# Kernel tuning notes

Hardware: AMD Instinct MI355X
Metric: run time of the kernel (lower is better)

The kernel has to match this reference:

```python
import jax, jax.numpy as jnp
import numpy as np

B, S, D = 16, 1024, 512
H, DH = 8, 64  # heads, dim_head


def setup_inputs() -> dict:
    key = jax.random.key(0)
    ks = jax.random.split(key, 7)
    x = jax.random.normal(ks[0], (B, S, D), dtype=jnp.float32)
    # variable sequence lengths in [1, S]
    seq_lens = jnp.maximum(jax.random.randint(ks[1], (B,), 0, S + 1), 1).astype(jnp.int32)
    w_std = 0.02
    Wq = jax.random.normal(ks[2], (D, D), dtype=jnp.float32) * w_std
    Wk = jax.random.normal(ks[3], (D, D), dtype=jnp.float32) * w_std
    Wv = jax.random.normal(ks[4], (D, D), dtype=jnp.float32) * w_std
    Wo = jax.random.normal(ks[5], (D, D), dtype=jnp.float32) * w_std
    bo = jnp.zeros((D,), dtype=jnp.float32)
    return {"x": x, "seq_lens": seq_lens, "Wq": Wq, "Wk": Wk, "Wv": Wv, "Wo": Wo, "bo": bo}


def reference(x, seq_lens, Wq, Wk, Wv, Wo, bo):
    # x: [B, S, D] padded ragged batch; seq_lens: [B] valid token counts.
    # Equivalent to the per-batch SDPA loop over jagged sequences: attention
    # is computed only among the valid tokens of each sequence.
    scale = DH ** -0.5
    q = (x @ Wq).reshape(B, S, H, DH)
    k = (x @ Wk).reshape(B, S, H, DH)
    v = (x @ Wv).reshape(B, S, H, DH)
    scores = jnp.einsum('bqhd,bkhd->bhqk', q, k) * scale  # [B,H,S,S]
    valid = jnp.arange(S)[None, :] < seq_lens[:, None]     # [B,S] token mask
    neg_inf = jnp.finfo(scores.dtype).min
    scores = jnp.where(valid[:, None, None, :], scores, neg_inf)
    attn = jax.nn.softmax(scores, axis=-1)
    out = jnp.einsum('bhqk,bkhd->bqhd', attn, v).reshape(B, S, D)
    out = out @ Wo + bo  # to_out Linear (dropout=0 / eval)
    return out * valid[:, :, None]  # zero padded query positions
```

## Files before the change

### kernel.cpp

```cpp
#include <hip/hip_runtime.h>
#include <hip/hip_bf16.h>

typedef __bf16 bf16_t;
typedef __attribute__((ext_vector_type(4))) __bf16 bf16x4;
typedef __attribute__((ext_vector_type(8))) __bf16 bf16x8;
typedef __attribute__((ext_vector_type(4))) float f32x4;

#define MFMA16(a, b, c) __builtin_amdgcn_mfma_f32_16x16x32_bf16((a), (b), (c), 0, 0, 0)

#define BB 16
#define SS 1024
#define DD 512
#define HH 8
#define DH 64
#define NTOK (BB * SS)
#define QSCALE 0.18033688f

typedef const __attribute__((address_space(1))) void gas_void;
typedef __attribute__((address_space(3))) void las_void;

__device__ __forceinline__ void async_cp16(const void* g, void* l) {
    __builtin_amdgcn_global_load_lds((gas_void*)g, (las_void*)l, 16, 0, 0);
}

__device__ __forceinline__ bf16x8 frag_ld(const char* sm, int row, int kk, int g) {
    int r7 = row & 7;
    int base = row * 128 + ((g & 1) << 3);
    int c0 = ((kk << 2) + (g >> 1)) ^ r7;
    int c1 = ((kk << 2) + 2 + (g >> 1)) ^ r7;
    bf16x4 lo = *(const bf16x4*)(sm + base + (c0 << 4));
    bf16x4 hi = *(const bf16x4*)(sm + base + (c1 << 4));
    return __builtin_shufflevector(lo, hi, 0, 1, 2, 3, 4, 5, 6, 7);
}

__device__ __forceinline__ bf16x8 fragl(const char* sm, int idx, int l) {
    return *(const bf16x8*)(sm + (idx * 64 + l) * 16);
}

__global__ __launch_bounds__(256) void cast_x_k(const float* __restrict__ x,
                                                bf16_t* __restrict__ xb, int n4) {
    int i = blockIdx.x * 256 + threadIdx.x;
    if (i < n4) {
        float4 v = ((const float4*)x)[i];
        bf16x4 o;
        o[0] = (bf16_t)v.x; o[1] = (bf16_t)v.y; o[2] = (bf16_t)v.z; o[3] = (bf16_t)v.w;
        *(bf16x4*)(xb + (size_t)i * 4) = o;
    }
}

__global__ __launch_bounds__(256) void transpose_w_k(const float* __restrict__ W0,
                                                     const float* __restrict__ W1,
                                                     const float* __restrict__ W2,
                                                     const float* __restrict__ W3,
                                                     bf16_t* __restrict__ Wt) {
    __shared__ float t[32][33];
    int z = blockIdx.z;
    const float* W = (z == 0) ? W0 : (z == 1) ? W1 : (z == 2) ? W2 : W3;
    bf16_t* out = Wt + (size_t)z * DD * DD;
    int n0 = blockIdx.x * 32, k0 = blockIdx.y * 32;
    int tx = threadIdx.x, ty = threadIdx.y;
#pragma unroll
    for (int i = 0; i < 32; i += 8)
        t[ty + i][tx] = W[(size_t)(k0 + ty + i) * DD + n0 + tx];
    __syncthreads();
#pragma unroll
    for (int i = 0; i < 32; i += 8)
        out[(size_t)(n0 + ty + i) * DD + k0 + tx] = (bf16_t)t[tx][ty + i];
}

__global__ void build_q_k(const int* __restrict__ sl, ushort* __restrict__ items,
                          int* __restrict__ meta) {
    int l = threadIdx.x;
    __shared__ int s_b[BB], s_cnt[BB], s_start[BB];
    if (l < BB) {
        int len = sl[l];
        int rank = 0;
        for (int j = 0; j < BB; ++j) {
            int lj = sl[j];
            if (lj > len || (lj == len && j < l)) ++rank;
        }
        s_b[rank] = l;
        s_cnt[rank] = ((len + 127) >> 7) * HH;
    }
    __syncthreads();
    if (l < BB) {
        int st = 0;
        for (int j = 0; j < l; ++j) st += s_cnt[j];
        s_start[l] = st;
        if (l == BB - 1) { meta[0] = st + s_cnt[l]; meta[1] = 0; }
    }
    __syncthreads();
    if (l < BB) {
        int b = s_b[l], st = s_start[l], c = s_cnt[l];
        int nqt = c >> 3;
        for (int i = 0; i < c; ++i) {
            int h = i / nqt, qt = i - h * nqt;
            items[st + i] = (ushort)((((b << 3) | h) << 3) | qt);
        }
    }
}

template <int MODE>
__global__ __launch_bounds__(256) void gemm_k(const bf16_t* __restrict__ A,
                                              const bf16_t* __restrict__ WtBase,
                                              bf16_t* __restrict__ oQ,
                                              bf16_t* __restrict__ oK,
                                              bf16_t* __restrict__ oVt,
                                              float* __restrict__ oO,
                                              const float* __restrict__ bo,
                                              const int* __restrict__ seq_lens) {
    __shared__ __align__(16) char smem[32768];
    char* smA = smem;
    char* smB = smem + 16384;
    const int tid = threadIdx.x;
    const int l = tid & 63, w = tid >> 6;
    const int lr = l & 15, g = l >> 4;
    const int bm = blockIdx.x, bn = blockIdx.y;
    const int z = (MODE == 0) ? blockIdx.z : 3;
    const bf16_t* Wt = WtBase + (size_t)z * DD * DD;
    const int row0 = bm * 128;
    const int col0 = bn * 128;
    const int wm = (w >> 1) * 64, wn = (w & 1) * 64;

    f32x4 acc[4][4] = {};

    for (int kt = 0; kt < 8; ++kt) {
        const int k0 = kt * 64;
        __syncthreads();
#pragma unroll
        for (int it = 0; it < 4; ++it) {
            int cl = it * 256 + tid;
            int m = cl >> 3, p = cl & 7, c = p ^ (m & 7);
            async_cp16(A + (size_t)(row0 + m) * DD + k0 + c * 8, smA + cl * 16);
        }
#pragma unroll
        for (int it = 0; it < 4; ++it) {
            int cl = it * 256 + tid;
            int m = cl >> 3, p = cl & 7, c = p ^ (m & 7);
            async_cp16(Wt + (size_t)(col0 + m) * DD + k0 + c * 8, smB + cl * 16);
        }
        __syncthreads();
#pragma unroll
        for (int kk = 0; kk < 2; ++kk) {
            bf16x8 af[4], bfr[4];
#pragma unroll
            for (int i = 0; i < 4; ++i) af[i] = frag_ld(smA, wm + i * 16 + lr, kk, g);
#pragma unroll
            for (int j = 0; j < 4; ++j) bfr[j] = frag_ld(smB, wn + j * 16 + lr, kk, g);
#pragma unroll
            for (int i = 0; i < 4; ++i)
#pragma unroll
                for (int j = 0; j < 4; ++j)
                    acc[i][j] = MFMA16(af[i], bfr[j], acc[i][j]);
        }
    }

    if (MODE == 0) {
        __syncthreads();
        char* tl = smem;
        const float sc = (z == 0) ? QSCALE : 1.f;
#pragma unroll
        for (int i = 0; i < 4; ++i)
#pragma unroll
            for (int j = 0; j < 4; ++j)
#pragma unroll
                for (int r = 0; r < 4; ++r) {
                    int s = wm + i * 16 + g * 4 + r;
                    int n = wn + j * 16 + lr;
                    int nb = 2 * n;
                    int byte = s * 256 + ((((nb >> 4) ^ (s & 7)) << 4) | (nb & 15));
                    *(bf16_t*)(tl + byte) = (bf16_t)(acc[i][j][r] * sc);
                }
        __syncthreads();
        const int b = row0 >> 10, s0 = row0 & 1023;
        if (z < 2) {
            bf16_t* dst = (z == 0) ? oQ : oK;
#pragma unroll
            for (int c8 = 0; c8 < 8; ++c8) {
                int combo = c8 * 4 + w;
                int kk = combo & 1, t = (combo >> 1) & 7, hl = combo >> 4;
                int s = 16 * t + lr;
                bf16x4 pr[2];
#pragma unroll
                for (int jj = 0; jj < 2; ++jj) {
                    int nb = 128 * hl + 64 * kk + 32 * jj + 8 * g;
                    int byte = s * 256 + ((((nb >> 4) ^ (s & 7)) << 4) | (nb & 15));
                    pr[jj] = *(const bf16x4*)(tl + byte);
                }
                bf16x8 v = __builtin_shufflevector(pr[0], pr[1], 0, 1, 2, 3, 4, 5, 6, 7);
                int bhh = b * 8 + (col0 >> 6) + hl;
                int tg = (s0 >> 4) + t;
                *(bf16x8*)(dst + (((size_t)bhh * 64 + tg) * 2 + kk) * 512 + l * 8) = v;
            }
        } else {
#pragma unroll
            for (int c8 = 0; c8 < 8; ++c8) {
                int combo = c8 * 4 + w;
                int kk = combo & 1, dt = (combo >> 1) & 3;
                int st = (combo >> 3) & 1, hl = (combo >> 4) & 1;
                bf16x8 v;
#pragma unroll
                for (int j = 0; j < 8; ++j) {
                    int s = 64 * st + 32 * kk + 16 * (j >> 2) + 4 * g + (j & 3);
                    int n = 64 * hl + 16 * dt + lr;
                    int nb = 2 * n;
                    int byte = s * 256 + ((((nb >> 4) ^ (s & 7)) << 4) | (nb & 15));
                    v[j] = *(const bf16_t*)(tl + byte);
                }
                int bhh = b * 8 + (col0 >> 6) + hl;
                int stg = (s0 >> 6) + st;
                *(bf16x8*)(oVt + ((((size_t)bhh * 16 + stg) * 4 + dt) * 2 + kk) * 512 +
                           l * 8) = v;
            }
        }
    } else {
        int b = row0 >> 10;
        int len = seq_lens[b];
#pragma unroll
        for (int i = 0; i < 4; ++i) {
            int mrow = row0 + wm + i * 16 + g * 4;
#pragma unroll
            for (int j = 0; j < 4; ++j) {
                int n = col0 + wn + j * 16 + lr;
                float bias = bo[n];
#pragma unroll
                for (int r = 0; r < 4; ++r) {
                    int m = mrow + r;
                    int s = m & 1023;
                    oO[(size_t)m * DD + n] = (s < len) ? (acc[i][j][r] + bias) : 0.f;
                }
            }
        }
    }
}

__global__ __launch_bounds__(256) void attn_k(const bf16_t* __restrict__ Qf,
                                              const bf16_t* __restrict__ Kf,
                                              const bf16_t* __restrict__ Vf,
                                              bf16_t* __restrict__ O,
                                              const int* __restrict__ seq_lens,
                                              const ushort* __restrict__ items,
                                              int* __restrict__ meta) {
    __shared__ __align__(16) char smem[49152];
    __shared__ int s_item;
    const int tid = threadIdx.x, l = tid & 63, w = tid >> 6;
    const int lr = l & 15, g = l >> 4;
    const int nitems = meta[0];
    int* cursor = meta + 1;

    for (;;) {
        if (tid == 0) s_item = atomicAdd(cursor, 1);
        __syncthreads();
        const int ii = s_item;
        if (ii >= nitems) return;
        const int itv = items[ii];
        const int qt = itv & 7, bh = itv >> 3;
        const int b = bh >> 3;
        const int len = seq_lens[b];
        const int q0 = qt * 128;
        const int h = bh & 7;

        const bf16_t* kfb = Kf + (size_t)bh * 65536;
        const bf16_t* vfb = Vf + (size_t)bh * 65536;

        bf16x8 bq[2][2];
#pragma unroll
        for (int qs = 0; qs < 2; ++qs) {
            int t = (q0 >> 4) + 2 * w + qs;
#pragma unroll
            for (int kk = 0; kk < 2; ++kk)
                bq[qs][kk] = *(const bf16x8*)(
                    Qf + (((size_t)bh * 64 + t) * 2 + kk) * 512 + l * 8);
        }

        f32x4 oacc[2][4] = {};
        float mrun[2] = {-1e30f, -1e30f};
        float lpart[2] = {0.f, 0.f};

        const int nkt = (len + 63) >> 6;

        auto stage = [&](int buf, int kti) {
            char* smK = smem + buf * 16384;
            char* smV = smK + 8192;
            const bf16_t* ks = kfb + kti * 4096;
            const bf16_t* vs = vfb + kti * 4096;
#pragma unroll
            for (int it = 0; it < 2; ++it) {
                int cl = it * 256 + tid;
                async_cp16(ks + cl * 8, smK + cl * 16);
            }
#pragma unroll
            for (int it = 0; it < 2; ++it) {
                int cl = it * 256 + tid;
                async_cp16(vs + cl * 8, smV + cl * 16);
            }
        };

        stage(0, 0);
        if (nkt > 1) stage(1, 1);
        int cur = 0;

        for (int kt = 0; kt < nkt; ++kt) {
            const int key0 = kt * 64;
            if (kt + 1 < nkt) {
                asm volatile("s_waitcnt vmcnt(4)" ::: "memory");
            } else {
                asm volatile("s_waitcnt vmcnt(0)" ::: "memory");
            }
            __builtin_amdgcn_s_barrier();
            __builtin_amdgcn_sched_barrier(0);
            if (kt + 2 < nkt) {
                int b2 = (cur >= 1) ? cur - 1 : 2;
                stage(b2, kt + 2);
            }
            const char* smK = smem + cur * 16384;
            const char* smV = smK + 8192;

            bf16x8 bv[4][2];
#pragma unroll
            for (int dt = 0; dt < 4; ++dt)
#pragma unroll
                for (int kk = 0; kk < 2; ++kk)
                    bv[dt][kk] = fragl(smV, dt * 2 + kk, l);

            f32x4 pacc[2][4] = {};
#pragma unroll
            for (int nt = 0; nt < 4; ++nt) {
                bf16x8 ak0 = fragl(smK, nt * 2 + 0, l);
                bf16x8 ak1 = fragl(smK, nt * 2 + 1, l);
#pragma unroll
                for (int qs = 0; qs < 2; ++qs) {
                    pacc[qs][nt] = MFMA16(ak0, bq[qs][0], pacc[qs][nt]);
                    pacc[qs][nt] = MFMA16(ak1, bq[qs][1], pacc[qs][nt]);
                }
            }

            const bool full = (key0 + 64 <= len);

#pragma unroll
            for (int qs = 0; qs < 2; ++qs) {
                float mloc = -1e30f;
                if (full) {
#pragma unroll
                    for (int nt = 0; nt < 4; ++nt)
#pragma unroll
                        for (int r = 0; r < 4; ++r) mloc = fmaxf(mloc, pacc[qs][nt][r]);
                } else {
#pragma unroll
                    for (int nt = 0; nt < 4; ++nt)
#pragma unroll
                        for (int r = 0; r < 4; ++r) {
                            int kg = key0 + nt * 16 + 4 * g + r;
                            float s = (kg < len) ? pacc[qs][nt][r] : -1e30f;
                            pacc[qs][nt][r] = s;
                            mloc = fmaxf(mloc, s);
                        }
                }
                mloc = fmaxf(mloc, __shfl_xor(mloc, 16, 64));
                mloc = fmaxf(mloc, __shfl_xor(mloc, 32, 64));

                float mn;
                if (__all(mloc <= mrun[qs])) {
                    mn = mrun[qs];
                } else {
                    mn = fmaxf(mrun[qs], mloc);
                    float corr = __builtin_amdgcn_exp2f(mrun[qs] - mn);
                    mrun[qs] = mn;
                    lpart[qs] *= corr;
                    float cb[4];
#pragma unroll
                    for (int r = 0; r < 4; ++r) cb[r] = __shfl(corr, 4 * g + r, 64);
#pragma unroll
                    for (int dt = 0; dt < 4; ++dt)
#pragma unroll
                        for (int r = 0; r < 4; ++r) oacc[qs][dt][r] *= cb[r];
                }

                float ls = 0.f;
#pragma unroll
                for (int nt = 0; nt < 4; ++nt)
#pragma unroll
                    for (int r = 0; r < 4; ++r) {
                        float p = __builtin_amdgcn_exp2f(pacc[qs][nt][r] - mn);
                        pacc[qs][nt][r] = p;
                        ls += p;
                    }
                lpart[qs] += ls;

                bf16x8 pa[2];
#pragma unroll
                for (int kf = 0; kf < 2; ++kf)
#pragma unroll
                    for (int j = 0; j < 8; ++j)
                        pa[kf][j] = (bf16_t)pacc[qs][2 * kf + (j >> 2)][j & 3];
#pragma unroll
                for (int kf = 0; kf < 2; ++kf)
#pragma unroll
                    for (int dt = 0; dt < 4; ++dt)
                        oacc[qs][dt] = MFMA16(pa[kf], bv[dt][kf], oacc[qs][dt]);
            }
            cur = (cur == 2) ? 0 : cur + 1;
        }

#pragma unroll
        for (int qs = 0; qs < 2; ++qs) {
            float lt = lpart[qs];
            lt += __shfl_xor(lt, 16, 64);
            lt += __shfl_xor(lt, 32, 64);
#pragma unroll
            for (int r = 0; r < 4; ++r) {
                float inv = 1.f / __shfl(lt, 4 * g + r, 64);
                int q = q0 + w * 32 + qs * 16 + 4 * g + r;
                size_t orow = ((size_t)b * SS + q) * DD;
#pragma unroll
                for (int dt = 0; dt < 4; ++dt)
                    O[orow + h * DH + dt * 16 + lr] = (bf16_t)(oacc[qs][dt][r] * inv);
            }
        }
    }
}

extern "C" void kernel_launch(void* const* d_in, const int* in_sizes, int n_in,
                              void* d_out, int out_size, void* d_ws, size_t ws_size,
                              hipStream_t stream) {
    const float* x = (const float*)d_in[0];
    const int* seq_lens = (const int*)d_in[1];
    const float* Wq = (const float*)d_in[2];
    const float* Wk = (const float*)d_in[3];
    const float* Wv = (const float*)d_in[4];
    const float* Wo = (const float*)d_in[5];
    const float* bo = (const float*)d_in[6];
    float* out = (float*)d_out;

    char* ws = (char*)d_ws;
    const size_t SEG = (size_t)NTOK * DD * sizeof(bf16_t);
    bf16_t* xb = (bf16_t*)ws;
    bf16_t* qb = (bf16_t*)(ws + SEG);
    bf16_t* kb = (bf16_t*)(ws + 2 * SEG);
    bf16_t* vtb = (bf16_t*)(ws + 3 * SEG);
    bf16_t* wt = (bf16_t*)(ws + 4 * SEG);
    ushort* items = (ushort*)(ws + 4 * SEG + (size_t)4 * DD * DD * sizeof(bf16_t));
    int* meta = (int*)(items + 1024);
    bf16_t* ab = xb;

    build_q_k<<<dim3(1), dim3(64), 0, stream>>>(seq_lens, items, meta);
    cast_x_k<<<dim3((NTOK * DD / 4) / 256), dim3(256), 0, stream>>>(x, xb, NTOK * DD / 4);
    transpose_w_k<<<dim3(16, 16, 4), dim3(32, 8), 0, stream>>>(Wq, Wk, Wv, Wo, wt);
    gemm_k<0><<<dim3(NTOK / 128, DD / 128, 3), dim3(256), 0, stream>>>(
        xb, wt, qb, kb, vtb, nullptr, nullptr, nullptr);
    attn_k<<<dim3(768), dim3(256), 0, stream>>>(qb, kb, vtb, ab, seq_lens, items, meta);
    gemm_k<2><<<dim3(NTOK / 128, DD / 128, 1), dim3(256), 0, stream>>>(
        ab, wt, nullptr, nullptr, nullptr, out, bo, seq_lens);
}
```

Baseline: 122.6 us.

## Make attention work items per-wave 32-query tiles with direct global K/V loads

The attention kernel now treats each wavefront as an independent worker. It pulls 32-query work items from the atomic queue with a wave-level shuffle instead of a block barrier, and reads K/V fragments straight from global memory into registers, dropping the LDS triple-buffered async staging. The finer items are meant to improve load balance across ragged sequence lengths and remove block-wide synchronisation. In exchange, K/V tiles are no longer shared across four waves through LDS, so global/L2 traffic roughly quadruples and load latency is no longer hidden by the prefetch pipeline.

Result: slower. 160.3 us (+30.8%).

```diff
diff --git a/kernel.cpp b/kernel.cpp
--- a/kernel.cpp
+++ b/kernel.cpp
@@ -31,10 +31,6 @@
     bf16x4 lo = *(const bf16x4*)(sm + base + (c0 << 4));
     bf16x4 hi = *(const bf16x4*)(sm + base + (c1 << 4));
     return __builtin_shufflevector(lo, hi, 0, 1, 2, 3, 4, 5, 6, 7);
-}
-
-__device__ __forceinline__ bf16x8 fragl(const char* sm, int idx, int l) {
-    return *(const bf16x8*)(sm + (idx * 64 + l) * 16);
 }
 
 __global__ __launch_bounds__(256) void cast_x_k(const float* __restrict__ x,
@@ -80,7 +76,7 @@
             if (lj > len || (lj == len && j < l)) ++rank;
         }
         s_b[rank] = l;
-        s_cnt[rank] = ((len + 127) >> 7) * HH;
+        s_cnt[rank] = ((len + 31) >> 5) * HH;
     }
     __syncthreads();
     if (l < BB) {
@@ -92,10 +88,10 @@
     __syncthreads();
     if (l < BB) {
         int b = s_b[l], st = s_start[l], c = s_cnt[l];
-        int nqt = c >> 3;
+        int nq32 = c >> 3;
         for (int i = 0; i < c; ++i) {
-            int h = i / nqt, qt = i - h * nqt;
-            items[st + i] = (ushort)((((b << 3) | h) << 3) | qt);
+            int h = i / nq32, qt = i - h * nq32;
+            items[st + i] = (ushort)((((b << 3) | h) << 5) | qt);
         }
     }
 }
@@ -241,37 +237,32 @@
                                               const int* __restrict__ seq_lens,
                                               const ushort* __restrict__ items,
                                               int* __restrict__ meta) {
-    __shared__ __align__(16) char smem[49152];
-    __shared__ int s_item;
-    const int tid = threadIdx.x, l = tid & 63, w = tid >> 6;
+    const int tid = threadIdx.x, l = tid & 63;
     const int lr = l & 15, g = l >> 4;
     const int nitems = meta[0];
     int* cursor = meta + 1;
 
     for (;;) {
-        if (tid == 0) s_item = atomicAdd(cursor, 1);
-        __syncthreads();
-        const int ii = s_item;
+        int v = 0;
+        if (l == 0) v = atomicAdd(cursor, 1);
+        const int ii = __shfl(v, 0, 64);
         if (ii >= nitems) return;
         const int itv = items[ii];
-        const int qt = itv & 7, bh = itv >> 3;
-        const int b = bh >> 3;
+        const int qt = itv & 31, bh = itv >> 5;
+        const int b = bh >> 3, h = bh & 7;
         const int len = seq_lens[b];
-        const int q0 = qt * 128;
-        const int h = bh & 7;
+        const int q0 = qt * 32;
 
         const bf16_t* kfb = Kf + (size_t)bh * 65536;
         const bf16_t* vfb = Vf + (size_t)bh * 65536;
 
         bf16x8 bq[2][2];
 #pragma unroll
-        for (int qs = 0; qs < 2; ++qs) {
-            int t = (q0 >> 4) + 2 * w + qs;
+        for (int qs = 0; qs < 2; ++qs)
 #pragma unroll
             for (int kk = 0; kk < 2; ++kk)
                 bq[qs][kk] = *(const bf16x8*)(
-                    Qf + (((size_t)bh * 64 + t) * 2 + kk) * 512 + l * 8);
-        }
+                    Qf + (((size_t)bh * 64 + (q0 >> 4) + qs) * 2 + kk) * 512 + l * 8);
 
         f32x4 oacc[2][4] = {};
         float mrun[2] = {-1e30f, -1e30f};
@@ -279,61 +270,32 @@
 
         const int nkt = (len + 63) >> 6;
 
-        auto stage = [&](int buf, int kti) {
-            char* smK = smem + buf * 16384;
-            char* smV = smK + 8192;
-            const bf16_t* ks = kfb + kti * 4096;
-            const bf16_t* vs = vfb + kti * 4096;
-#pragma unroll
-            for (int it = 0; it < 2; ++it) {
-                int cl = it * 256 + tid;
-                async_cp16(ks + cl * 8, smK + cl * 16);
-            }
-#pragma unroll
-            for (int it = 0; it < 2; ++it) {
-                int cl = it * 256 + tid;
-                async_cp16(vs + cl * 8, smV + cl * 16);
-            }
-        };
-
-        stage(0, 0);
-        if (nkt > 1) stage(1, 1);
-        int cur = 0;
-
         for (int kt = 0; kt < nkt; ++kt) {
             const int key0 = kt * 64;
-            if (kt + 1 < nkt) {
-                asm volatile("s_waitcnt vmcnt(4)" ::: "memory");
-            } else {
-                asm volatile("s_waitcnt vmcnt(0)" ::: "memory");
-            }
-            __builtin_amdgcn_s_barrier();
-            __builtin_amdgcn_sched_barrier(0);
-            if (kt + 2 < nkt) {
-                int b2 = (cur >= 1) ? cur - 1 : 2;
-                stage(b2, kt + 2);
-            }
-            const char* smK = smem + cur * 16384;
-            const char* smV = smK + 8192;
+            bf16x8 ak[4][2];
+#pragma unroll
+            for (int nt = 0; nt < 4; ++nt)
+#pragma unroll
+                for (int kk = 0; kk < 2; ++kk)
+                    ak[nt][kk] = *(const bf16x8*)(
+                        kfb + (size_t)((kt * 4 + nt) * 2 + kk) * 512 + l * 8);
+
+            f32x4 pacc[2][4] = {};
+#pragma unroll
+            for (int nt = 0; nt < 4; ++nt)
+#pragma unroll
+                for (int qs = 0; qs < 2; ++qs) {
+                    pacc[qs][nt] = MFMA16(ak[nt][0], bq[qs][0], pacc[qs][nt]);
+                    pacc[qs][nt] = MFMA16(ak[nt][1], bq[qs][1], pacc[qs][nt]);
+                }
 
             bf16x8 bv[4][2];
 #pragma unroll
             for (int dt = 0; dt < 4; ++dt)
 #pragma unroll
                 for (int kk = 0; kk < 2; ++kk)
-                    bv[dt][kk] = fragl(smV, dt * 2 + kk, l);
-
-            f32x4 pacc[2][4] = {};
-#pragma unroll
-            for (int nt = 0; nt < 4; ++nt) {
-                bf16x8 ak0 = fragl(smK, nt * 2 + 0, l);
-                bf16x8 ak1 = fragl(smK, nt * 2 + 1, l);
-#pragma unroll
-                for (int qs = 0; qs < 2; ++qs) {
-                    pacc[qs][nt] = MFMA16(ak0, bq[qs][0], pacc[qs][nt]);
-                    pacc[qs][nt] = MFMA16(ak1, bq[qs][1], pacc[qs][nt]);
-                }
-            }
+                    bv[dt][kk] = *(const bf16x8*)(
+                        vfb + (size_t)((kt * 8) + dt * 2 + kk) * 512 + l * 8);
 
             const bool full = (key0 + 64 <= len);
 
@@ -399,7 +361,6 @@
                     for (int dt = 0; dt < 4; ++dt)
                         oacc[qs][dt] = MFMA16(pa[kf], bv[dt][kf], oacc[qs][dt]);
             }
-            cur = (cur == 2) ? 0 : cur + 1;
         }
 
 #pragma unroll
@@ -410,7 +371,7 @@
 #pragma unroll
             for (int r = 0; r < 4; ++r) {
                 float inv = 1.f / __shfl(lt, 4 * g + r, 64);
-                int q = q0 + w * 32 + qs * 16 + 4 * g + r;
+                int q = q0 + qs * 16 + 4 * g + r;
                 size_t orow = ((size_t)b * SS + q) * DD;
 #pragma unroll
                 for (int dt = 0; dt < 4; ++dt)
@@ -440,7 +401,7 @@
     bf16_t* vtb = (bf16_t*)(ws + 3 * SEG);
     bf16_t* wt = (bf16_t*)(ws + 4 * SEG);
     ushort* items = (ushort*)(ws + 4 * SEG + (size_t)4 * DD * DD * sizeof(bf16_t));
-    int* meta = (int*)(items + 1024);
+    int* meta = (int*)(items + 4096);
     bf16_t* ab = xb;
 
     build_q_k<<<dim3(1), dim3(64), 0, stream>>>(seq_lens, items, meta);
@@ -448,7 +409,7 @@
     transpose_w_k<<<dim3(16, 16, 4), dim3(32, 8), 0, stream>>>(Wq, Wk, Wv, Wo, wt);
     gemm_k<0><<<dim3(NTOK / 128, DD / 128, 3), dim3(256), 0, stream>>>(
         xb, wt, qb, kb, vtb, nullptr, nullptr, nullptr);
-    attn_k<<<dim3(768), dim3(256), 0, stream>>>(qb, kb, vtb, ab, seq_lens, items, meta);
+    attn_k<<<dim3(512), dim3(256), 0, stream>>>(qb, kb, vtb, ab, seq_lens, items, meta);
     gemm_k<2><<<dim3(NTOK / 128, DD / 128, 1), dim3(256), 0, stream>>>(
         ab, wt, nullptr, nullptr, nullptr, out, bo, seq_lens);
 }
```

## Shrink attention query tile to 64 rows, double-buffer K/V, lazy rescale

Applied to the files above, without the earlier changes.

Attention work items now cover 64 query rows per head (16 per wave) instead of 128, so the persistent scheduler has finer-grained items and less padding for ragged lengths, and the grid grows to 1280 blocks. K/V staging moves from a 3-deep to a 2-deep LDS ring with full waitcnt, which cuts shared memory to 32 KB but exposes more load latency. The online softmax now rescales only when the new max exceeds the running max by more than 8 (in log2 units), which skips correction work but lets exponentials grow up to 2^8 before normalization. Each wave now reuses every K/V fragment read from LDS for only one 16-row query tile instead of two, raising LDS traffic per FLOP.

Measured after the change: 126.4 us. 3.1% more time.

```diff
diff --git a/kernel.cpp b/kernel.cpp
--- a/kernel.cpp
+++ b/kernel.cpp
@@ -80,7 +80,7 @@
             if (lj > len || (lj == len && j < l)) ++rank;
         }
         s_b[rank] = l;
-        s_cnt[rank] = ((len + 127) >> 7) * HH;
+        s_cnt[rank] = ((len + 63) >> 6) * HH;
     }
     __syncthreads();
     if (l < BB) {
@@ -92,10 +92,10 @@
     __syncthreads();
     if (l < BB) {
         int b = s_b[l], st = s_start[l], c = s_cnt[l];
-        int nqt = c >> 3;
+        int nq = c >> 3;
         for (int i = 0; i < c; ++i) {
-            int h = i / nqt, qt = i - h * nqt;
-            items[st + i] = (ushort)((((b << 3) | h) << 3) | qt);
+            int h = i / nq, qt = i - h * nq;
+            items[st + i] = (ushort)((((b << 3) | h) << 4) | qt);
         }
     }
 }
@@ -241,7 +241,7 @@
                                               const int* __restrict__ seq_lens,
                                               const ushort* __restrict__ items,
                                               int* __restrict__ meta) {
-    __shared__ __align__(16) char smem[49152];
+    __shared__ __align__(16) char smem[32768];
     __shared__ int s_item;
     const int tid = threadIdx.x, l = tid & 63, w = tid >> 6;
     const int lr = l & 15, g = l >> 4;
@@ -254,28 +254,23 @@
         const int ii = s_item;
         if (ii >= nitems) return;
         const int itv = items[ii];
-        const int qt = itv & 7, bh = itv >> 3;
-        const int b = bh >> 3;
+        const int qt = itv & 15, bh = itv >> 4;
+        const int b = bh >> 3, h = bh & 7;
         const int len = seq_lens[b];
-        const int q0 = qt * 128;
-        const int h = bh & 7;
+        const int q0 = qt * 64 + w * 16;
 
         const bf16_t* kfb = Kf + (size_t)bh * 65536;
         const bf16_t* vfb = Vf + (size_t)bh * 65536;
 
-        bf16x8 bq[2][2];
-#pragma unroll
-        for (int qs = 0; qs < 2; ++qs) {
-            int t = (q0 >> 4) + 2 * w + qs;
-#pragma unroll
-            for (int kk = 0; kk < 2; ++kk)
-                bq[qs][kk] = *(const bf16x8*)(
-                    Qf + (((size_t)bh * 64 + t) * 2 + kk) * 512 + l * 8);
-        }
-
-        f32x4 oacc[2][4] = {};
-        float mrun[2] = {-1e30f, -1e30f};
-        float lpart[2] = {0.f, 0.f};
+        bf16x8 bq[2];
+        {
+            size_t tb = ((size_t)bh * 64 + (q0 >> 4)) * 2;
+            bq[0] = *(const bf16x8*)(Qf + (tb + 0) * 512 + l * 8);
+            bq[1] = *(const bf16x8*)(Qf + (tb + 1) * 512 + l * 8);
+        }
+
+        f32x4 oacc[4] = {};
+        float mrun = -1e30f, lpart = 0.f;
 
         const int nkt = (len + 63) >> 6;
 
@@ -284,137 +279,107 @@
             char* smV = smK + 8192;
             const bf16_t* ks = kfb + kti * 4096;
             const bf16_t* vs = vfb + kti * 4096;
-#pragma unroll
-            for (int it = 0; it < 2; ++it) {
-                int cl = it * 256 + tid;
-                async_cp16(ks + cl * 8, smK + cl * 16);
-            }
-#pragma unroll
-            for (int it = 0; it < 2; ++it) {
-                int cl = it * 256 + tid;
-                async_cp16(vs + cl * 8, smV + cl * 16);
-            }
+            async_cp16(ks + tid * 8, smK + tid * 16);
+            async_cp16(ks + (256 + tid) * 8, smK + (256 + tid) * 16);
+            async_cp16(vs + tid * 8, smV + tid * 16);
+            async_cp16(vs + (256 + tid) * 8, smV + (256 + tid) * 16);
         };
 
         stage(0, 0);
-        if (nkt > 1) stage(1, 1);
         int cur = 0;
 
         for (int kt = 0; kt < nkt; ++kt) {
             const int key0 = kt * 64;
-            if (kt + 1 < nkt) {
-                asm volatile("s_waitcnt vmcnt(4)" ::: "memory");
-            } else {
-                asm volatile("s_waitcnt vmcnt(0)" ::: "memory");
-            }
+            asm volatile("s_waitcnt vmcnt(0)" ::: "memory");
             __builtin_amdgcn_s_barrier();
-            __builtin_amdgcn_sched_barrier(0);
-            if (kt + 2 < nkt) {
-                int b2 = (cur >= 1) ? cur - 1 : 2;
-                stage(b2, kt + 2);
-            }
+            if (kt + 1 < nkt) stage(cur ^ 1, kt + 1);
             const char* smK = smem + cur * 16384;
             const char* smV = smK + 8192;
 
-            bf16x8 bv[4][2];
-#pragma unroll
-            for (int dt = 0; dt < 4; ++dt)
-#pragma unroll
-                for (int kk = 0; kk < 2; ++kk)
-                    bv[dt][kk] = fragl(smV, dt * 2 + kk, l);
-
-            f32x4 pacc[2][4] = {};
+            f32x4 pacc[4] = {};
 #pragma unroll
             for (int nt = 0; nt < 4; ++nt) {
                 bf16x8 ak0 = fragl(smK, nt * 2 + 0, l);
                 bf16x8 ak1 = fragl(smK, nt * 2 + 1, l);
-#pragma unroll
-                for (int qs = 0; qs < 2; ++qs) {
-                    pacc[qs][nt] = MFMA16(ak0, bq[qs][0], pacc[qs][nt]);
-                    pacc[qs][nt] = MFMA16(ak1, bq[qs][1], pacc[qs][nt]);
-                }
+                pacc[nt] = MFMA16(ak0, bq[0], pacc[nt]);
+                pacc[nt] = MFMA16(ak1, bq[1], pacc[nt]);
             }
 
             const bool full = (key0 + 64 <= len);
 
-#pragma unroll
-            for (int qs = 0; qs < 2; ++qs) {
-                float mloc = -1e30f;
-                if (full) {
-#pragma unroll
-                    for (int nt = 0; nt < 4; ++nt)
-#pragma unroll
-                        for (int r = 0; r < 4; ++r) mloc = fmaxf(mloc, pacc[qs][nt][r]);
-                } else {
-#pragma unroll
-                    for (int nt = 0; nt < 4; ++nt)
-#pragma unroll
-                        for (int r = 0; r < 4; ++r) {
-                            int kg = key0 + nt * 16 + 4 * g + r;
-                            float s = (kg < len) ? pacc[qs][nt][r] : -1e30f;
-                            pacc[qs][nt][r] = s;
-                            mloc = fmaxf(mloc, s);
-                        }
-                }
-                mloc = fmaxf(mloc, __shfl_xor(mloc, 16, 64));
-                mloc = fmaxf(mloc, __shfl_xor(mloc, 32, 64));
-
-                float mn;
-                if (__all(mloc <= mrun[qs])) {
-                    mn = mrun[qs];
-                } else {
-                    mn = fmaxf(mrun[qs], mloc);
-                    float corr = __builtin_amdgcn_exp2f(mrun[qs] - mn);
-                    mrun[qs] = mn;
-                    lpart[qs] *= corr;
-                    float cb[4];
-#pragma unroll
-                    for (int r = 0; r < 4; ++r) cb[r] = __shfl(corr, 4 * g + r, 64);
-#pragma unroll
-                    for (int dt = 0; dt < 4; ++dt)
-#pragma unroll
-                        for (int r = 0; r < 4; ++r) oacc[qs][dt][r] *= cb[r];
-                }
-
-                float ls = 0.f;
+            float mloc = -1e30f;
+            if (full) {
 #pragma unroll
                 for (int nt = 0; nt < 4; ++nt)
 #pragma unroll
+                    for (int r = 0; r < 4; ++r) mloc = fmaxf(mloc, pacc[nt][r]);
+            } else {
+#pragma unroll
+                for (int nt = 0; nt < 4; ++nt)
+#pragma unroll
                     for (int r = 0; r < 4; ++r) {
-                        float p = __builtin_amdgcn_exp2f(pacc[qs][nt][r] - mn);
-                        pacc[qs][nt][r] = p;
-                        ls += p;
+                        int kg = key0 + nt * 16 + 4 * g + r;
+                        float s = (kg < len) ? pacc[nt][r] : -1e30f;
+                        pacc[nt][r] = s;
+                        mloc = fmaxf(mloc, s);
                     }
-                lpart[qs] += ls;
-
-                bf16x8 pa[2];
-#pragma unroll
-                for (int kf = 0; kf < 2; ++kf)
-#pragma unroll
-                    for (int j = 0; j < 8; ++j)
-                        pa[kf][j] = (bf16_t)pacc[qs][2 * kf + (j >> 2)][j & 3];
-#pragma unroll
-                for (int kf = 0; kf < 2; ++kf)
-#pragma unroll
-                    for (int dt = 0; dt < 4; ++dt)
-                        oacc[qs][dt] = MFMA16(pa[kf], bv[dt][kf], oacc[qs][dt]);
-            }
-            cur = (cur == 2) ? 0 : cur + 1;
-        }
-
-#pragma unroll
-        for (int qs = 0; qs < 2; ++qs) {
-            float lt = lpart[qs];
+            }
+            mloc = fmaxf(mloc, __shfl_xor(mloc, 16, 64));
+            mloc = fmaxf(mloc, __shfl_xor(mloc, 32, 64));
+
+            if (!__all(mloc <= mrun + 8.f)) {
+                float mn = fmaxf(mrun, mloc);
+                float corr = __builtin_amdgcn_exp2f(mrun - mn);
+                mrun = mn;
+                lpart *= corr;
+                float cb[4];
+#pragma unroll
+                for (int r = 0; r < 4; ++r) cb[r] = __shfl(corr, 4 * g + r, 64);
+#pragma unroll
+                for (int dt = 0; dt < 4; ++dt)
+#pragma unroll
+                    for (int r = 0; r < 4; ++r) oacc[dt][r] *= cb[r];
+            }
+
+            float ls = 0.f;
+#pragma unroll
+            for (int nt = 0; nt < 4; ++nt)
+#pragma unroll
+                for (int r = 0; r < 4; ++r) {
+                    float p = __builtin_amdgcn_exp2f(pacc[nt][r] - mrun);
+                    pacc[nt][r] = p;
+                    ls += p;
+                }
+            lpart += ls;
+
+            bf16x8 pa[2];
+#pragma unroll
+            for (int kf = 0; kf < 2; ++kf)
+#pragma unroll
+                for (int j = 0; j < 8; ++j)
+                    pa[kf][j] = (bf16_t)pacc[2 * kf + (j >> 2)][j & 3];
+#pragma unroll
+            for (int kf = 0; kf < 2; ++kf)
+#pragma unroll
+                for (int dt = 0; dt < 4; ++dt) {
+                    bf16x8 bv = fragl(smV, dt * 2 + kf, l);
+                    oacc[dt] = MFMA16(pa[kf], bv, oacc[dt]);
+                }
+            cur ^= 1;
+        }
+
+        {
+            float lt = lpart;
             lt += __shfl_xor(lt, 16, 64);
             lt += __shfl_xor(lt, 32, 64);
 #pragma unroll
             for (int r = 0; r < 4; ++r) {
                 float inv = 1.f / __shfl(lt, 4 * g + r, 64);
-                int q = q0 + w * 32 + qs * 16 + 4 * g + r;
+                int q = q0 + 4 * g + r;
                 size_t orow = ((size_t)b * SS + q) * DD;
 #pragma unroll
                 for (int dt = 0; dt < 4; ++dt)
-                    O[orow + h * DH + dt * 16 + lr] = (bf16_t)(oacc[qs][dt][r] * inv);
+                    O[orow + h * DH + dt * 16 + lr] = (bf16_t)(oacc[dt][r] * inv);
             }
         }
     }
@@ -440,7 +405,7 @@
     bf16_t* vtb = (bf16_t*)(ws + 3 * SEG);
     bf16_t* wt = (bf16_t*)(ws + 4 * SEG);
     ushort* items = (ushort*)(ws + 4 * SEG + (size_t)4 * DD * DD * sizeof(bf16_t));
-    int* meta = (int*)(items + 1024);
+    int* meta = (int*)(items + 4096);
     bf16_t* ab = xb;
 
     build_q_k<<<dim3(1), dim3(64), 0, stream>>>(seq_lens, items, meta);
@@ -448,7 +413,7 @@
     transpose_w_k<<<dim3(16, 16, 4), dim3(32, 8), 0, stream>>>(Wq, Wk, Wv, Wo, wt);
     gemm_k<0><<<dim3(NTOK / 128, DD / 128, 3), dim3(256), 0, stream>>>(
         xb, wt, qb, kb, vtb, nullptr, nullptr, nullptr);
-    attn_k<<<dim3(768), dim3(256), 0, stream>>>(qb, kb, vtb, ab, seq_lens, items, meta);
+    attn_k<<<dim3(1280), dim3(256), 0, stream>>>(qb, kb, vtb, ab, seq_lens, items, meta);
     gemm_k<2><<<dim3(NTOK / 128, DD / 128, 1), dim3(256), 0, stream>>>(
         ab, wt, nullptr, nullptr, nullptr, out, bo, seq_lens);
 }
```
